# Performance work log

Measured on AMD Instinct MI355X. Metric: run time of the kernel, lower is better.

## Reference

```python
import jax, jax.numpy as jnp
import numpy as np

B, N, DIM, H = 8, 1024, 1024, 16
D = DIM // H  # head dim = 64
SCALE = DIM ** (-0.5)  # NOTE: original uses full dim, not head dim


def setup_inputs() -> dict:
    key = jax.random.key(0)
    ks = jax.random.split(key, 8)
    x = jax.random.normal(ks[0], (B, N, DIM), dtype=jnp.float32)
    pos = jax.random.normal(ks[1], (B, N, DIM), dtype=jnp.float32)
    mask = jax.random.bernoulli(ks[2], 0.9, (B, N - 1))  # bool, [b, n-1]
    w_std = 0.02
    W_qk = jax.random.normal(ks[3], (2 * DIM, DIM), dtype=jnp.float32) * w_std  # Linear(dim, 2*dim_qk)
    W_v = jax.random.normal(ks[4], (DIM, DIM), dtype=jnp.float32) * w_std
    W_out = jax.random.normal(ks[5], (DIM, DIM), dtype=jnp.float32) * w_std
    b_out = jax.random.normal(ks[6], (DIM,), dtype=jnp.float32) * w_std
    return {"x": x, "mask": mask, "pos": pos, "W_qk": W_qk, "W_v": W_v,
            "W_out": W_out, "b_out": b_out}


def _split_heads(t):
    # b n (h d) -> b h n d
    b, n, _ = t.shape
    return t.reshape(b, n, H, D).transpose(0, 2, 1, 3)


def reference(x, mask, pos, W_qk, W_v, W_out, b_out):
    qk = x @ W_qk.T                       # [b, n, 2*dim]
    q, k = jnp.split(qk, 2, axis=-1)
    v = x @ W_v.T                         # [b, n, dim]
    q, k, v = _split_heads(q), _split_heads(k), _split_heads(v)  # [b,h,n,d]
    hpos = _split_heads(pos)
    q = q + hpos
    k = k + hpos
    dots = jnp.einsum('bhid,bhjd->bhij', q, k) * SCALE  # [b,h,n,n]
    mask_value = -jnp.finfo(dots.dtype).max
    # pad mask with True at position 0 (CLS token always visible)
    m = jnp.pad(mask, ((0, 0), (1, 0)), constant_values=True)  # [b, n]
    m2 = m[:, None, :] & m[:, :, None]                          # [b, n, n]
    dots = jnp.where(m2[:, None, :, :], dots, mask_value)
    attn = jax.nn.softmax(dots, axis=-1)
    out = jnp.einsum('bhij,bhjd->bhid', attn, v)  # [b,h,n,d]
    out = out.transpose(0, 2, 1, 3).reshape(x.shape[0], x.shape[1], DIM)  # b n (h d)
    out = out @ W_out.T + b_out  # dropout p=0.0 -> identity
    return out
```

## Files before the change

### kernel.cpp

```cpp
#include <hip/hip_runtime.h>


typedef unsigned short u16;
typedef short bf16x8 __attribute__((ext_vector_type(8)));
typedef float f32x4 __attribute__((ext_vector_type(4)));
typedef float f32x16 __attribute__((ext_vector_type(16)));
typedef int i32x2 __attribute__((ext_vector_type(2)));

#define MFMA16(a, b, c) __builtin_amdgcn_mfma_f32_16x16x32_bf16((a), (b), (c), 0, 0, 0)
#define MFMA32(a, b, c) __builtin_amdgcn_mfma_f32_32x32x16_bf16((a), (b), (c), 0, 0, 0)

__device__ __forceinline__ u16 f2bf(float f) {
    union { float f; unsigned u; } x; x.f = f;
    unsigned r = x.u + 0x7fffu + ((x.u >> 16) & 1u);
    return (u16)(r >> 16);
}

__device__ __forceinline__ void gld16(const u16* g, u16* l) {
    __builtin_amdgcn_global_load_lds(
        (const __attribute__((address_space(1))) void*)g,
        (__attribute__((address_space(3))) void*)l, 16, 0, 0);
}

__global__ __launch_bounds__(256) void cast_all(
    const float* __restrict__ x, const float* __restrict__ wqk,
    const float* __restrict__ wv, const float* __restrict__ wout,
    u16* __restrict__ xbf, u16* __restrict__ wqkvbf, u16* __restrict__ woutbf) {
    int i = blockIdx.x * 256 + threadIdx.x;
    const float* src; u16* dst; int off;
    if (i < 2097152)      { src = x;    dst = xbf;              off = i; }
    else if (i < 2621440) { src = wqk;  dst = wqkvbf;           off = i - 2097152; }
    else if (i < 2883584) { src = wv;   dst = wqkvbf + 2097152; off = i - 2621440; }
    else                  { src = wout; dst = woutbf;           off = i - 2883584; }
    float4 v = ((const float4*)src)[off];
    ushort4 o;
    o.x = f2bf(v.x); o.y = f2bf(v.y); o.z = f2bf(v.z); o.w = f2bf(v.w);
    ((ushort4*)dst)[off] = o;
}

#define GEMM_STAGE(c, k0_, PA, PB)                                                     \
    do {                                                                               \
        _Pragma("unroll")                                                              \
        for (int p = 0; p < 4; ++p) {                                                  \
            int rbase = w * 32 + p * 8;                                                \
            gld16((PA) + (size_t)(m0 + rbase + sr) * 1024 + (k0_) + scx,               \
                  &SS[c][0][rbase * 64]);                                              \
            gld16((PB) + (size_t)(n0 + rbase + sr) * 1024 + (k0_) + scx,               \
                  &SS[c][1][rbase * 64]);                                              \
        }                                                                              \
    } while (0)

__global__ __launch_bounds__(256) void gemm_qk(
    const u16* __restrict__ A,
    const u16* __restrict__ Bw,
    const float* __restrict__ pos,
    u16* __restrict__ Q, u16* __restrict__ Kx) {
    const int n0 = blockIdx.x * 128, m0 = blockIdx.y * 128;
    const int t = threadIdx.x, w = t >> 6, ln = t & 63;
    const int l15 = ln & 15, l4 = ln >> 4;
    const int wm = (w >> 1) * 64, wn = (w & 1) * 64;

    __shared__ u16 SS[2][2][128 * 64];

    f32x4 acc[4][4];
#pragma unroll
    for (int i = 0; i < 4; ++i)
#pragma unroll
        for (int j = 0; j < 4; ++j) acc[i][j] = (f32x4){0.f, 0.f, 0.f, 0.f};

    const int sr = ln >> 3;
    const int scx = ((ln & 7) ^ sr) * 8;
    const int x0 = (l15 & 7);

    GEMM_STAGE(0, 0, A, Bw);
    int cur = 0;
    for (int k0 = 0; k0 < 1024; k0 += 64) {
        if (k0 < 960) {
            GEMM_STAGE(cur ^ 1, k0 + 64, A, Bw);
            asm volatile("s_waitcnt vmcnt(8)" ::: "memory");
        } else {
            asm volatile("s_waitcnt vmcnt(0)" ::: "memory");
        }
        __builtin_amdgcn_s_barrier();
        const u16* Asb = SS[cur][0];
        const u16* Bsb = SS[cur][1];
#pragma unroll
        for (int kt = 0; kt < 2; ++kt) {
            bf16x8 a[4], bfr[4];
#pragma unroll
            for (int mt = 0; mt < 4; ++mt)
                a[mt] = *(const bf16x8*)&Asb[(wm + mt * 16 + l15) * 64 + ((kt * 4 + l4) ^ x0) * 8];
#pragma unroll
            for (int nt = 0; nt < 4; ++nt)
                bfr[nt] = *(const bf16x8*)&Bsb[(wn + nt * 16 + l15) * 64 + ((kt * 4 + l4) ^ x0) * 8];
#pragma unroll
            for (int mt = 0; mt < 4; ++mt)
#pragma unroll
                for (int nt = 0; nt < 4; ++nt)
                    acc[mt][nt] = MFMA16(a[mt], bfr[nt], acc[mt][nt]);
        }
        __builtin_amdgcn_sched_barrier(0);
        __builtin_amdgcn_s_barrier();
        cur ^= 1;
    }
#pragma unroll
    for (int mt = 0; mt < 4; ++mt)
#pragma unroll
        for (int nt = 0; nt < 4; ++nt)
#pragma unroll
            for (int r = 0; r < 4; ++r) {
                int i = m0 + wm + mt * 16 + l4 * 4 + r;
                int j = n0 + wn + nt * 16 + l15;
                int bb = i >> 10, n = i & 1023;
                int jj = j & 1023;
                float v = acc[mt][nt][r] + pos[(size_t)i * 1024 + jj];
                int hh = jj >> 6, dd = jj & 63;
                size_t idx = (((size_t)(bb * 16 + hh)) * 1024 + n) * 64 + dd;
                if (j < 1024) Q[idx] = f2bf(v * 0.045084220027780106f);
                else          Kx[idx] = f2bf(v);
            }
}

__global__ __launch_bounds__(256) void zero_k(
    const int* __restrict__ maskIn,
    u16* __restrict__ Kx) {
    int tid = blockIdx.x * 256 + threadIdx.x;
    int seg = tid & 7;
    int row = tid >> 3;
    int n = row & 1023;
    int b = row >> 14;
    if (n == 0) return;
    if (maskIn[b * 1023 + n - 1] != 0) return;
    uint4 z = {0u, 0u, 0u, 0u};
    *(uint4*)(Kx + (size_t)row * 64 + seg * 8) = z;
}

__global__ __launch_bounds__(256) void gemm_v(
    const u16* __restrict__ Wv,
    const u16* __restrict__ X,
    u16* __restrict__ Vt) {
    const int n0 = blockIdx.x * 128, m0 = blockIdx.y * 128;
    const int bIdx = blockIdx.z;
    const u16* Xb = X + (size_t)bIdx * 1048576;
    const int t = threadIdx.x, w = t >> 6, ln = t & 63;
    const int l15 = ln & 15, l4 = ln >> 4;
    const int wm = (w >> 1) * 64, wn = (w & 1) * 64;

    __shared__ u16 SS[2][2][128 * 64];

    f32x4 acc[4][4];
#pragma unroll
    for (int i = 0; i < 4; ++i)
#pragma unroll
        for (int j = 0; j < 4; ++j) acc[i][j] = (f32x4){0.f, 0.f, 0.f, 0.f};

    const int sr = ln >> 3;
    const int scx = ((ln & 7) ^ sr) * 8;
    const int x0 = (l15 & 7);

    GEMM_STAGE(0, 0, Wv, Xb);
    int cur = 0;
    for (int k0 = 0; k0 < 1024; k0 += 64) {
        if (k0 < 960) {
            GEMM_STAGE(cur ^ 1, k0 + 64, Wv, Xb);
            asm volatile("s_waitcnt vmcnt(8)" ::: "memory");
        } else {
            asm volatile("s_waitcnt vmcnt(0)" ::: "memory");
        }
        __builtin_amdgcn_s_barrier();
        const u16* Asb = SS[cur][0];
        const u16* Bsb = SS[cur][1];
#pragma unroll
        for (int kt = 0; kt < 2; ++kt) {
            bf16x8 a[4], bfr[4];
#pragma unroll
            for (int mt = 0; mt < 4; ++mt)
                a[mt] = *(const bf16x8*)&Asb[(wm + mt * 16 + l15) * 64 + ((kt * 4 + l4) ^ x0) * 8];
#pragma unroll
            for (int nt = 0; nt < 4; ++nt)
                bfr[nt] = *(const bf16x8*)&Bsb[(wn + nt * 16 + l15) * 64 + ((kt * 4 + l4) ^ x0) * 8];
#pragma unroll
            for (int mt = 0; mt < 4; ++mt)
#pragma unroll
                for (int nt = 0; nt < 4; ++nt)
                    acc[mt][nt] = MFMA16(a[mt], bfr[nt], acc[mt][nt]);
        }
        __builtin_amdgcn_sched_barrier(0);
        __builtin_amdgcn_s_barrier();
        cur ^= 1;
    }
#pragma unroll
    for (int mt = 0; mt < 4; ++mt)
#pragma unroll
        for (int nt = 0; nt < 4; ++nt)
#pragma unroll
            for (int r = 0; r < 4; ++r) {
                int i = m0 + wm + mt * 16 + l4 * 4 + r;
                int j = n0 + wn + nt * 16 + l15;
                Vt[((size_t)(bIdx * 1024 + i)) * 1024 + j] = f2bf(acc[mt][nt][r]);
            }
}

__global__ __launch_bounds__(64) void vsum_kernel(const u16* __restrict__ Vt,
                                                  const int* __restrict__ maskIn,
                                                  float* __restrict__ Vsum,
                                                  float* __restrict__ Vmask) {
    int row = blockIdx.x, ln = threadIdx.x;
    int b = row >> 10;
    const u16* p = Vt + (size_t)row * 1024 + ln * 16;
    uint4 a = *(const uint4*)p;
    uint4 bq = *(const uint4*)(p + 8);
    float s = 0.f, sm = 0.f;
    unsigned vv[8] = {a.x, a.y, a.z, a.w, bq.x, bq.y, bq.z, bq.w};
#pragma unroll
    for (int i = 0; i < 8; ++i) {
        int j0 = ln * 16 + 2 * i;
        float lo = __uint_as_float(vv[i] << 16);
        float hi = __uint_as_float(vv[i] & 0xffff0000u);
        s += lo + hi;
        bool ok0 = (j0 == 0) || (maskIn[b * 1023 + j0 - 1] != 0);
        bool ok1 = (maskIn[b * 1023 + j0] != 0);
        if (!ok0) sm += lo;
        if (!ok1) sm += hi;
    }
#pragma unroll
    for (int d = 1; d < 64; d <<= 1) { s += __shfl_xor(s, d); sm += __shfl_xor(sm, d); }
    if (ln == 0) { Vsum[row] = s; Vmask[row] = sm; }
}

__global__ __launch_bounds__(512) void attn_kernel(
    const u16* __restrict__ Q,
    const u16* __restrict__ Kx,
    const u16* __restrict__ Vt,
    const int* __restrict__ maskIn,
    const float* __restrict__ Vsum,
    const float* __restrict__ Vmask,
    u16* __restrict__ O) {
    const int gid = blockIdx.x;
    const int bh = gid & 127;
    const int qt = gid >> 7;
    const int b = bh >> 4, h = bh & 15;
    const int t = threadIdx.x, w = t >> 6, ln = t & 63;
    const int half = w >> 2, wq = w & 3;
    const int l31 = ln & 31, l5 = ln >> 5;

    __shared__ __align__(16) char lds[73760];
    float* nm = (float*)(lds + 73728);
    u16* KsBase = (u16*)(lds + half * 36864);

    {
        float cnt = 0.f;
        for (int i = t; i < 1023; i += 512)
            cnt += (maskIn[b * 1023 + i] == 0) ? 1.f : 0.f;
#pragma unroll
        for (int d = 1; d < 64; d <<= 1) cnt += __shfl_xor(cnt, d);
        if (ln == 0) nm[w] = cnt;
    }

    const size_t qkbase = (size_t)bh * 65536;
    const int q0 = qt * 128 + wq * 32;
    const int q = q0 + l31;

    bf16x8 bq[4];
#pragma unroll
    for (int kt = 0; kt < 4; ++kt)
        bq[kt] = *(const bf16x8*)(Q + qkbase + (size_t)q * 64 + kt * 16 + l5 * 8);

    float lsum = 0.f;
    f32x16 o0 = {0,0,0,0,0,0,0,0,0,0,0,0,0,0,0,0};
    f32x16 o1 = {0,0,0,0,0,0,0,0,0,0,0,0,0,0,0,0};

    const int th = t & 255;
    const int srow = th >> 2, sc = (th & 3) * 16;
    const int jbase = half * 512;

    uint4 kv, kv2, vv, vv2;
#define ALOAD(j0_)                                                                      \
    do {                                                                                \
        kv  = *(const uint4*)(Kx + qkbase + (size_t)((j0_) + srow) * 64 + sc);          \
        kv2 = *(const uint4*)(Kx + qkbase + (size_t)((j0_) + srow) * 64 + sc + 8);      \
        vv  = *(const uint4*)(Vt + qkbase + (size_t)srow * 1024 + (j0_) + sc);          \
        vv2 = *(const uint4*)(Vt + qkbase + (size_t)srow * 1024 + (j0_) + sc + 8);      \
    } while (0)
#define AWRITE(c)                                                                       \
    do {                                                                                \
        u16* Ksw = KsBase + (c) * 9216;                                                 \
        u16* Vsw = Ksw + 4608;                                                          \
        *(uint4*)&Ksw[srow * 72 + sc] = kv;                                             \
        *(uint4*)&Ksw[srow * 72 + sc + 8] = kv2;                                        \
        *(uint4*)&Vsw[srow * 72 + sc] = vv;                                             \
        *(uint4*)&Vsw[srow * 72 + sc + 8] = vv2;                                        \
    } while (0)

    ALOAD(jbase);
    AWRITE(0);
    ALOAD(jbase + 64);
    __syncthreads();

    int cur = 0;
    for (int jt = 0; jt < 8; ++jt) {
        const u16* Ks = KsBase + cur * 9216;
        const u16* Vs = Ks + 4608;

        f32x16 st0 = {0,0,0,0,0,0,0,0,0,0,0,0,0,0,0,0};
        f32x16 st1 = {0,0,0,0,0,0,0,0,0,0,0,0,0,0,0,0};
        __builtin_amdgcn_s_setprio(1);
#pragma unroll
        for (int ktk = 0; ktk < 4; ++ktk) {
            bf16x8 ak0 = *(const bf16x8*)&Ks[(l31) * 72 + ktk * 16 + l5 * 8];
            bf16x8 ak1 = *(const bf16x8*)&Ks[(32 + l31) * 72 + ktk * 16 + l5 * 8];
            st0 = MFMA32(ak0, bq[ktk], st0);
            st1 = MFMA32(ak1, bq[ktk], st1);
        }
        __builtin_amdgcn_s_setprio(0);
#pragma unroll
        for (int i = 0; i < 16; ++i) {
            float p0 = __builtin_amdgcn_exp2f(st0[i]);
            float p1 = __builtin_amdgcn_exp2f(st1[i]);
            st0[i] = p0;
            st1[i] = p1;
            lsum += p0 + p1;
        }
        unsigned pk0[8], pk1[8];
#pragma unroll
        for (int g = 0; g < 4; ++g) {
#pragma unroll
            for (int qq = 0; qq < 2; ++qq) {
                unsigned r0, r1;
                asm("v_cvt_pk_bf16_f32 %0, %1, %2"
                    : "=v"(r0) : "v"(st0[g * 4 + 2 * qq]), "v"(st0[g * 4 + 2 * qq + 1]));
                asm("v_cvt_pk_bf16_f32 %0, %1, %2"
                    : "=v"(r1) : "v"(st1[g * 4 + 2 * qq]), "v"(st1[g * 4 + 2 * qq + 1]));
                pk0[2 * g + qq] = r0;
                pk1[2 * g + qq] = r1;
            }
        }
        bf16x8 pf[4];
#pragma unroll
        for (int kt = 0; kt < 4; ++kt) {
            const int hh = kt & 1;
            unsigned wa0 = (kt < 2) ? pk0[4 * hh]     : pk1[4 * hh];
            unsigned wa1 = (kt < 2) ? pk0[4 * hh + 1] : pk1[4 * hh + 1];
            unsigned wb0 = (kt < 2) ? pk0[4 * hh + 2] : pk1[4 * hh + 2];
            unsigned wb1 = (kt < 2) ? pk0[4 * hh + 3] : pk1[4 * hh + 3];
            i32x2 s02 = __builtin_amdgcn_permlane32_swap((int)wa0, (int)wb0, false, false);
            i32x2 s13 = __builtin_amdgcn_permlane32_swap((int)wa1, (int)wb1, false, false);
            union { unsigned u[4]; bf16x8 v; } cv;
            cv.u[0] = (unsigned)s02.x;
            cv.u[1] = (unsigned)s13.x;
            cv.u[2] = (unsigned)s02.y;
            cv.u[3] = (unsigned)s13.y;
            pf[kt] = cv.v;
        }
        __builtin_amdgcn_s_setprio(1);
#pragma unroll
        for (int kt = 0; kt < 4; ++kt) {
            bf16x8 av0 = *(const bf16x8*)&Vs[(l31) * 72 + kt * 16 + l5 * 8];
            bf16x8 av1 = *(const bf16x8*)&Vs[(32 + l31) * 72 + kt * 16 + l5 * 8];
            o0 = MFMA32(av0, pf[kt], o0);
            o1 = MFMA32(av1, pf[kt], o1);
        }
        __builtin_amdgcn_s_setprio(0);

        if (jt < 7) {
            AWRITE(cur ^ 1);
            if (jt < 6) ALOAD(jbase + (jt + 2) * 64);
        }
        __builtin_amdgcn_sched_barrier(0);
        __syncthreads();
        cur ^= 1;
    }
#undef ALOAD
#undef AWRITE

    float* comb = (float*)lds;
    if (half == 1) {
        float* dst = comb + ((size_t)(wq * 64 + ln)) * 33;
#pragma unroll
        for (int i = 0; i < 16; ++i) { dst[i] = o0[i]; dst[16 + i] = o1[i]; }
        dst[32] = lsum;
    }
    __syncthreads();
    if (half == 0) {
        const float* src = comb + ((size_t)(wq * 64 + ln)) * 33;
#pragma unroll
        for (int i = 0; i < 16; ++i) { o0[i] += src[i]; o1[i] += src[16 + i]; }
        lsum += src[32];
        float lrow = lsum + __shfl_xor(lsum, 32);
        float nmaskb = nm[0] + nm[1] + nm[2] + nm[3] + nm[4] + nm[5] + nm[6] + nm[7];
        lrow -= nmaskb;
        const float linv = 1.f / lrow;
        const int n = q0 + l31;
        const bool rqv = (n == 0) || (maskIn[b * 1023 + n - 1] != 0);
        u16* orow = O + ((size_t)(b * 1024 + n)) * 1024 + h * 64;
#pragma unroll
        for (int g = 0; g < 4; ++g) {
            ushort4 s0, s1;
            unsigned short* p0 = (unsigned short*)&s0;
            unsigned short* p1 = (unsigned short*)&s1;
#pragma unroll
            for (int r = 0; r < 4; ++r) {
                int reg = 4 * g + r;
                int d0 = 8 * g + 4 * l5 + r;
                float v0 = rqv ? (o0[reg] - Vmask[bh * 64 + d0]) * linv
                               : Vsum[bh * 64 + d0] * 0.0009765625f;
                float v1 = rqv ? (o1[reg] - Vmask[bh * 64 + 32 + d0]) * linv
                               : Vsum[bh * 64 + 32 + d0] * 0.0009765625f;
                p0[r] = f2bf(v0);
                p1[r] = f2bf(v1);
            }
            *(ushort4*)&orow[8 * g + 4 * l5] = s0;
            *(ushort4*)&orow[32 + 8 * g + 4 * l5] = s1;
        }
    }
}

__global__ __launch_bounds__(256) void gemm_out(
    const u16* __restrict__ A,
    const u16* __restrict__ Bw,
    const float* __restrict__ bias,
    float* __restrict__ out) {
    const int n0 = blockIdx.x * 128, m0 = blockIdx.y * 128;
    const int t = threadIdx.x, w = t >> 6, ln = t & 63;
    const int l15 = ln & 15, l4 = ln >> 4;
    const int wm = (w >> 1) * 64, wn = (w & 1) * 64;

    __shared__ u16 SS[2][2][128 * 64];

    f32x4 acc[4][4];
#pragma unroll
    for (int i = 0; i < 4; ++i)
#pragma unroll
        for (int j = 0; j < 4; ++j) acc[i][j] = (f32x4){0.f, 0.f, 0.f, 0.f};

    const int sr = ln >> 3;
    const int scx = ((ln & 7) ^ sr) * 8;
    const int x0 = (l15 & 7);

    GEMM_STAGE(0, 0, A, Bw);
    int cur = 0;
    for (int k0 = 0; k0 < 1024; k0 += 64) {
        if (k0 < 960) {
            GEMM_STAGE(cur ^ 1, k0 + 64, A, Bw);
            asm volatile("s_waitcnt vmcnt(8)" ::: "memory");
        } else {
            asm volatile("s_waitcnt vmcnt(0)" ::: "memory");
        }
        __builtin_amdgcn_s_barrier();
        const u16* Asb = SS[cur][0];
        const u16* Bsb = SS[cur][1];
#pragma unroll
        for (int kt = 0; kt < 2; ++kt) {
            bf16x8 a[4], bfr[4];
#pragma unroll
            for (int mt = 0; mt < 4; ++mt)
                a[mt] = *(const bf16x8*)&Asb[(wm + mt * 16 + l15) * 64 + ((kt * 4 + l4) ^ x0) * 8];
#pragma unroll
            for (int nt = 0; nt < 4; ++nt)
                bfr[nt] = *(const bf16x8*)&Bsb[(wn + nt * 16 + l15) * 64 + ((kt * 4 + l4) ^ x0) * 8];
#pragma unroll
            for (int mt = 0; mt < 4; ++mt)
#pragma unroll
                for (int nt = 0; nt < 4; ++nt)
                    acc[mt][nt] = MFMA16(a[mt], bfr[nt], acc[mt][nt]);
        }
        __builtin_amdgcn_sched_barrier(0);
        __builtin_amdgcn_s_barrier();
        cur ^= 1;
    }
#pragma unroll
    for (int mt = 0; mt < 4; ++mt)
#pragma unroll
        for (int nt = 0; nt < 4; ++nt)
#pragma unroll
            for (int r = 0; r < 4; ++r) {
                int i = m0 + wm + mt * 16 + l4 * 4 + r;
                int j = n0 + wn + nt * 16 + l15;
                out[(size_t)i * 1024 + j] = acc[mt][nt][r] + bias[j];
            }
}

extern "C" void kernel_launch(void* const* d_in, const int* in_sizes, int n_in,
                              void* d_out, int out_size, void* d_ws, size_t ws_size,
                              hipStream_t stream) {
    const float* x    = (const float*)d_in[0];
    const int*   mask = (const int*)d_in[1];
    const float* pos  = (const float*)d_in[2];
    const float* wqk  = (const float*)d_in[3];
    const float* wv   = (const float*)d_in[4];
    const float* wout = (const float*)d_in[5];
    const float* bout = (const float*)d_in[6];

    char* ws = (char*)d_ws;
    u16* xbf    = (u16*)(ws + 0);
    u16* wqkvbf = (u16*)(ws + 16777216);
    u16* woutbf = (u16*)(ws + 23068672);
    u16* Qb     = (u16*)(ws + 25165824);
    u16* Kb     = (u16*)(ws + 41943040);
    u16* Vtb    = (u16*)(ws + 58720256);
    float* Vsum = (float*)(ws + 16777216);
    float* Vmask = (float*)(ws + 16777216 + 32768);

    cast_all<<<12288, 256, 0, stream>>>(x, wqk, wv, wout, xbf, wqkvbf, woutbf);

    gemm_qk<<<dim3(16, 64), 256, 0, stream>>>(xbf, wqkvbf, pos, Qb, Kb);
    zero_k<<<4096, 256, 0, stream>>>(mask, Kb);
    gemm_v<<<dim3(8, 8, 8), 256, 0, stream>>>(wqkvbf + 2097152, xbf, Vtb);
    vsum_kernel<<<8192, 64, 0, stream>>>(Vtb, mask, Vsum, Vmask);
    attn_kernel<<<1024, 512, 0, stream>>>(Qb, Kb, Vtb, mask, Vsum, Vmask, xbf);
    gemm_out<<<dim3(8, 64), 256, 0, stream>>>(xbf, woutbf, bout, (float*)d_out);
}
```

Before: 279.7 us.

## Fuse Q/K/V projection GEMMs and merge K-zeroing with V-sum kernels

Merges the separate QK and V projection GEMMs into one launch over a 24-column tile grid. V tiles write transposed output directly with ushort4 stores. The zero_k and vsum kernels are combined into a single fixup launch that packs four rows per 256-thread block. Block indices are also swizzled in the QKV and output GEMMs so neighbouring blocks share the same A rows and get better L2 reuse. The aim is fewer launches and better cache locality, at the cost of a transposed V store pattern with strided writes.

Result: faster. 270.1 us (-3.4%).

```diff
diff --git a/kernel.cpp b/kernel.cpp
--- a/kernel.cpp
+++ b/kernel.cpp
@@ -50,12 +50,14 @@
         }                                                                              \
     } while (0)
 
-__global__ __launch_bounds__(256) void gemm_qk(
+__global__ __launch_bounds__(256) void gemm_qkv(
     const u16* __restrict__ A,
     const u16* __restrict__ Bw,
     const float* __restrict__ pos,
-    u16* __restrict__ Q, u16* __restrict__ Kx) {
-    const int n0 = blockIdx.x * 128, m0 = blockIdx.y * 128;
+    u16* __restrict__ Q, u16* __restrict__ Kx, u16* __restrict__ Vt) {
+    const int lid = blockIdx.x;
+    const int swz = (lid & 7) * 192 + (lid >> 3);
+    const int n0 = (swz % 24) * 128, m0 = (swz / 24) * 128;
     const int t = threadIdx.x, w = t >> 6, ln = t & 63;
     const int l15 = ln & 15, l4 = ln >> 4;
     const int wm = (w >> 1) * 64, wn = (w & 1) * 64;
@@ -103,129 +105,80 @@
         __builtin_amdgcn_s_barrier();
         cur ^= 1;
     }
-#pragma unroll
-    for (int mt = 0; mt < 4; ++mt)
-#pragma unroll
-        for (int nt = 0; nt < 4; ++nt)
-#pragma unroll
-            for (int r = 0; r < 4; ++r) {
-                int i = m0 + wm + mt * 16 + l4 * 4 + r;
-                int j = n0 + wn + nt * 16 + l15;
-                int bb = i >> 10, n = i & 1023;
-                int jj = j & 1023;
-                float v = acc[mt][nt][r] + pos[(size_t)i * 1024 + jj];
-                int hh = jj >> 6, dd = jj & 63;
-                size_t idx = (((size_t)(bb * 16 + hh)) * 1024 + n) * 64 + dd;
-                if (j < 1024) Q[idx] = f2bf(v * 0.045084220027780106f);
-                else          Kx[idx] = f2bf(v);
+    if (n0 < 2048) {
+#pragma unroll
+        for (int mt = 0; mt < 4; ++mt)
+#pragma unroll
+            for (int nt = 0; nt < 4; ++nt)
+#pragma unroll
+                for (int r = 0; r < 4; ++r) {
+                    int i = m0 + wm + mt * 16 + l4 * 4 + r;
+                    int j = n0 + wn + nt * 16 + l15;
+                    int bb = i >> 10, n = i & 1023;
+                    int jj = j & 1023;
+                    float v = acc[mt][nt][r] + pos[(size_t)i * 1024 + jj];
+                    int hh = jj >> 6, dd = jj & 63;
+                    size_t idx = (((size_t)(bb * 16 + hh)) * 1024 + n) * 64 + dd;
+                    if (j < 1024) Q[idx] = f2bf(v * 0.045084220027780106f);
+                    else          Kx[idx] = f2bf(v);
+                }
+    } else {
+#pragma unroll
+        for (int mt = 0; mt < 4; ++mt)
+#pragma unroll
+            for (int nt = 0; nt < 4; ++nt) {
+                const int i0 = m0 + wm + mt * 16 + l4 * 4;
+                const int bb = i0 >> 10, n = i0 & 1023;
+                const int vfull = (n0 - 2048) + wn + nt * 16 + l15;
+                ushort4 s;
+                unsigned short* sp = (unsigned short*)&s;
+#pragma unroll
+                for (int r = 0; r < 4; ++r) sp[r] = f2bf(acc[mt][nt][r]);
+                *(ushort4*)&Vt[((size_t)(bb * 1024 + vfull)) * 1024 + n] = s;
             }
-}
-
-__global__ __launch_bounds__(256) void zero_k(
+    }
+}
+
+__global__ __launch_bounds__(256) void fixup(
     const int* __restrict__ maskIn,
-    u16* __restrict__ Kx) {
-    int tid = blockIdx.x * 256 + threadIdx.x;
-    int seg = tid & 7;
-    int row = tid >> 3;
-    int n = row & 1023;
-    int b = row >> 14;
-    if (n == 0) return;
-    if (maskIn[b * 1023 + n - 1] != 0) return;
-    uint4 z = {0u, 0u, 0u, 0u};
-    *(uint4*)(Kx + (size_t)row * 64 + seg * 8) = z;
-}
-
-__global__ __launch_bounds__(256) void gemm_v(
-    const u16* __restrict__ Wv,
-    const u16* __restrict__ X,
-    u16* __restrict__ Vt) {
-    const int n0 = blockIdx.x * 128, m0 = blockIdx.y * 128;
-    const int bIdx = blockIdx.z;
-    const u16* Xb = X + (size_t)bIdx * 1048576;
-    const int t = threadIdx.x, w = t >> 6, ln = t & 63;
-    const int l15 = ln & 15, l4 = ln >> 4;
-    const int wm = (w >> 1) * 64, wn = (w & 1) * 64;
-
-    __shared__ u16 SS[2][2][128 * 64];
-
-    f32x4 acc[4][4];
-#pragma unroll
-    for (int i = 0; i < 4; ++i)
-#pragma unroll
-        for (int j = 0; j < 4; ++j) acc[i][j] = (f32x4){0.f, 0.f, 0.f, 0.f};
-
-    const int sr = ln >> 3;
-    const int scx = ((ln & 7) ^ sr) * 8;
-    const int x0 = (l15 & 7);
-
-    GEMM_STAGE(0, 0, Wv, Xb);
-    int cur = 0;
-    for (int k0 = 0; k0 < 1024; k0 += 64) {
-        if (k0 < 960) {
-            GEMM_STAGE(cur ^ 1, k0 + 64, Wv, Xb);
-            asm volatile("s_waitcnt vmcnt(8)" ::: "memory");
-        } else {
-            asm volatile("s_waitcnt vmcnt(0)" ::: "memory");
-        }
-        __builtin_amdgcn_s_barrier();
-        const u16* Asb = SS[cur][0];
-        const u16* Bsb = SS[cur][1];
-#pragma unroll
-        for (int kt = 0; kt < 2; ++kt) {
-            bf16x8 a[4], bfr[4];
-#pragma unroll
-            for (int mt = 0; mt < 4; ++mt)
-                a[mt] = *(const bf16x8*)&Asb[(wm + mt * 16 + l15) * 64 + ((kt * 4 + l4) ^ x0) * 8];
-#pragma unroll
-            for (int nt = 0; nt < 4; ++nt)
-                bfr[nt] = *(const bf16x8*)&Bsb[(wn + nt * 16 + l15) * 64 + ((kt * 4 + l4) ^ x0) * 8];
-#pragma unroll
-            for (int mt = 0; mt < 4; ++mt)
-#pragma unroll
-                for (int nt = 0; nt < 4; ++nt)
-                    acc[mt][nt] = MFMA16(a[mt], bfr[nt], acc[mt][nt]);
-        }
-        __builtin_amdgcn_sched_barrier(0);
-        __builtin_amdgcn_s_barrier();
-        cur ^= 1;
-    }
-#pragma unroll
-    for (int mt = 0; mt < 4; ++mt)
-#pragma unroll
-        for (int nt = 0; nt < 4; ++nt)
-#pragma unroll
-            for (int r = 0; r < 4; ++r) {
-                int i = m0 + wm + mt * 16 + l4 * 4 + r;
-                int j = n0 + wn + nt * 16 + l15;
-                Vt[((size_t)(bIdx * 1024 + i)) * 1024 + j] = f2bf(acc[mt][nt][r]);
-            }
-}
-
-__global__ __launch_bounds__(64) void vsum_kernel(const u16* __restrict__ Vt,
-                                                  const int* __restrict__ maskIn,
-                                                  float* __restrict__ Vsum,
-                                                  float* __restrict__ Vmask) {
-    int row = blockIdx.x, ln = threadIdx.x;
-    int b = row >> 10;
-    const u16* p = Vt + (size_t)row * 1024 + ln * 16;
-    uint4 a = *(const uint4*)p;
-    uint4 bq = *(const uint4*)(p + 8);
-    float s = 0.f, sm = 0.f;
-    unsigned vv[8] = {a.x, a.y, a.z, a.w, bq.x, bq.y, bq.z, bq.w};
-#pragma unroll
-    for (int i = 0; i < 8; ++i) {
-        int j0 = ln * 16 + 2 * i;
-        float lo = __uint_as_float(vv[i] << 16);
-        float hi = __uint_as_float(vv[i] & 0xffff0000u);
-        s += lo + hi;
-        bool ok0 = (j0 == 0) || (maskIn[b * 1023 + j0 - 1] != 0);
-        bool ok1 = (maskIn[b * 1023 + j0] != 0);
-        if (!ok0) sm += lo;
-        if (!ok1) sm += hi;
-    }
-#pragma unroll
-    for (int d = 1; d < 64; d <<= 1) { s += __shfl_xor(s, d); sm += __shfl_xor(sm, d); }
-    if (ln == 0) { Vsum[row] = s; Vmask[row] = sm; }
+    u16* __restrict__ Kx,
+    const u16* __restrict__ Vt,
+    float* __restrict__ Vsum, float* __restrict__ Vmask) {
+    const int bid = blockIdx.x;
+    if (bid < 4096) {
+        int tid = bid * 256 + threadIdx.x;
+        int seg = tid & 7;
+        int row = tid >> 3;
+        int n = row & 1023;
+        int b = row >> 14;
+        if (n == 0) return;
+        if (maskIn[b * 1023 + n - 1] != 0) return;
+        uint4 z = {0u, 0u, 0u, 0u};
+        *(uint4*)(Kx + (size_t)row * 64 + seg * 8) = z;
+    } else {
+        int w = threadIdx.x >> 6, ln = threadIdx.x & 63;
+        int row = (bid - 4096) * 4 + w;
+        int b = row >> 10;
+        const u16* p = Vt + (size_t)row * 1024 + ln * 16;
+        uint4 a = *(const uint4*)p;
+        uint4 bq = *(const uint4*)(p + 8);
+        float s = 0.f, sm = 0.f;
+        unsigned vv[8] = {a.x, a.y, a.z, a.w, bq.x, bq.y, bq.z, bq.w};
+#pragma unroll
+        for (int i = 0; i < 8; ++i) {
+            int j0 = ln * 16 + 2 * i;
+            float lo = __uint_as_float(vv[i] << 16);
+            float hi = __uint_as_float(vv[i] & 0xffff0000u);
+            s += lo + hi;
+            bool ok0 = (j0 == 0) || (maskIn[b * 1023 + j0 - 1] != 0);
+            bool ok1 = (maskIn[b * 1023 + j0] != 0);
+            if (!ok0) sm += lo;
+            if (!ok1) sm += hi;
+        }
+#pragma unroll
+        for (int d = 1; d < 64; d <<= 1) { s += __shfl_xor(s, d); sm += __shfl_xor(sm, d); }
+        if (ln == 0) { Vsum[row] = s; Vmask[row] = sm; }
+    }
 }
 
 __global__ __launch_bounds__(512) void attn_kernel(
@@ -420,7 +373,9 @@
     const u16* __restrict__ Bw,
     const float* __restrict__ bias,
     float* __restrict__ out) {
-    const int n0 = blockIdx.x * 128, m0 = blockIdx.y * 128;
+    const int lid = blockIdx.x;
+    const int swz = (lid & 7) * 64 + (lid >> 3);
+    const int n0 = (swz % 8) * 128, m0 = (swz / 8) * 128;
     const int t = threadIdx.x, w = t >> 6, ln = t & 63;
     const int l15 = ln & 15, l4 = ln >> 4;
     const int wm = (w >> 1) * 64, wn = (w & 1) * 64;
@@ -503,10 +458,8 @@
 
     cast_all<<<12288, 256, 0, stream>>>(x, wqk, wv, wout, xbf, wqkvbf, woutbf);
 
-    gemm_qk<<<dim3(16, 64), 256, 0, stream>>>(xbf, wqkvbf, pos, Qb, Kb);
-    zero_k<<<4096, 256, 0, stream>>>(mask, Kb);
-    gemm_v<<<dim3(8, 8, 8), 256, 0, stream>>>(wqkvbf + 2097152, xbf, Vtb);
-    vsum_kernel<<<8192, 64, 0, stream>>>(Vtb, mask, Vsum, Vmask);
+    gemm_qkv<<<1536, 256, 0, stream>>>(xbf, wqkvbf, pos, Qb, Kb, Vtb);
+    fixup<<<6144, 256, 0, stream>>>(mask, Kb, Vtb, Vsum, Vmask);
     attn_kernel<<<1024, 512, 0, stream>>>(Qb, Kb, Vtb, mask, Vsum, Vmask, xbf);
-    gemm_out<<<dim3(8, 64), 256, 0, stream>>>(xbf, woutbf, bout, (float*)d_out);
-}
+    gemm_out<<<512, 256, 0, stream>>>(xbf, woutbf, bout, (float*)d_out);
+}
```
